# Performance work log

Measured on AMD Instinct MI355X. Metric: run time of the kernel, lower is better.

The kernel has to match this reference:

```python
import jax, jax.numpy as jnp
import numpy as np

LOG2PI = float(np.log(2.0 * np.pi))
CLIP_LO, CLIP_HI = 1e-6, 1.0 - 1e-6


def gaussian_log_prob(X, mu):
    # X: (s, d), mu: (K, d) -> (s, K); unit-variance diagonal Normal.
    d = X.shape[-1]
    sq = (
        (X * X).sum(-1, keepdims=True)
        - 2.0 * (X @ mu.T)
        + (mu * mu).sum(-1)[None, :]
    )
    return -0.5 * (sq + d * LOG2PI)


def setup_inputs() -> dict:
    key = jax.random.key(0)
    kz, ks, kd, km1, km2 = jax.random.split(key, 5)
    s, K, n, dz = 60000, 200, 6, 64
    Z = jax.random.normal(kz, (s, dz), dtype=jnp.float32)
    S = jax.random.normal(ks, (s, 3), dtype=jnp.float32)
    D = jax.random.randint(kd, (s, n), 0, s, dtype=jnp.int64)
    sel_mu = jax.random.normal(km1, (K, dz), dtype=jnp.float32)
    spa_mu = jax.random.normal(km2, (K, 3), dtype=jnp.float32)
    return {"Z": Z, "S": S, "D": D, "sel_mu": sel_mu, "spa_mu": spa_mu}


def reference(Z, S, D, sel_mu, spa_mu):
    # point energy U: (s, K)
    U = -(gaussian_log_prob(Z, sel_mu) + gaussian_log_prob(S, spa_mu))
    Q = jax.nn.softmax(-U, axis=-1)  # temperature = 1.0
    # expected point energy: (s,)
    point = (Q * U).sum(-1)
    # doublet energy: gather neighbor rows, coassignment, potential, mask
    Qc = jnp.clip(Q, CLIP_LO, CLIP_HI)
    co = jnp.einsum('snk,sk->sn', Qc[D], Qc)  # (s, n)
    doublet = jnp.where(D < 0, 0.0, -jnp.log(co)).sum(-1)  # (s,)
    return point + doublet
```

## Files before the change

kernel.cpp:

```cpp
#include <hip/hip_runtime.h>
#include <hip/hip_fp16.h>
#include <math.h>

#define KK 200
#define NT 13
#define NNB 6
#define Q8STRIDE 256

typedef __attribute__((ext_vector_type(8))) short short8;
typedef __attribute__((ext_vector_type(4))) float f32x4;
#define MFMA16 __builtin_amdgcn_mfma_f32_16x16x32_bf16

__device__ __forceinline__ unsigned short bfh(float f) {
    unsigned u = __float_as_uint(f);
    return (unsigned short)((u + 0x7fffu + ((u >> 16) & 1u)) >> 16);
}
__device__ __forceinline__ float bf2f(unsigned short h) {
    return __uint_as_float(((unsigned)h) << 16);
}
__device__ __forceinline__ short8 z8() {
    short8 v;
#pragma unroll
    for (int j = 0; j < 8; ++j) v[j] = 0;
    return v;
}
__device__ __forceinline__ void cv2(float f, short8& hi, short8& lo, int j) {
    unsigned short h = bfh(f);
    hi[j] = (short)h;
    lo[j] = (short)bfh(f - bf2f(h));
}
__device__ __forceinline__ unsigned f2e5(float f) {
    unsigned short hb = __half_as_ushort(__float2half(f));
    return (unsigned)((unsigned short)((hb + 0x7fu + ((hb >> 8) & 1u)) >> 8));
}
__device__ __forceinline__ void dec8(unsigned w, float* f) {
    f[0] = __half2float(__ushort_as_half((unsigned short)((w << 8) & 0xff00u)));
    f[1] = __half2float(__ushort_as_half((unsigned short)(w & 0xff00u)));
    f[2] = __half2float(__ushort_as_half((unsigned short)((w >> 8) & 0xff00u)));
    f[3] = __half2float(__ushort_as_half((unsigned short)((w >> 16) & 0xff00u)));
}

__global__ __launch_bounds__(512, 4) void
k_point(const float* __restrict__ Z, const float* __restrict__ S,
        const float* __restrict__ selmu, const float* __restrict__ spamu,
        unsigned char* __restrict__ Qc8, float* __restrict__ pointbuf,
        int sRows, int mTiles)
{
    __shared__ short8 ldsBh[26 * 64];
    __shared__ short8 ldsBl[26 * 64];
    __shared__ uint2  ldsB2h[NT * 16];
    __shared__ uint2  ldsB2l[NT * 16];

    const int tid = threadIdx.x;

    for (int slot = tid; slot < 26 * 64; slot += 512) {
        int L = slot & 63, ts = slot >> 6;
        int t = ts >> 1, sstep = ts & 1;
        int n = t * 16 + (L & 15);
        int kb = sstep * 32 + (L >> 4) * 8;
        short8 hi = z8(), lo = z8();
        if (n < KK) {
            const float* mp = selmu + (size_t)n * 64 + kb;
            float4 a = *(const float4*)mp;
            float4 b = *(const float4*)(mp + 4);
            cv2(a.x, hi, lo, 0); cv2(a.y, hi, lo, 1); cv2(a.z, hi, lo, 2); cv2(a.w, hi, lo, 3);
            cv2(b.x, hi, lo, 4); cv2(b.y, hi, lo, 5); cv2(b.z, hi, lo, 6); cv2(b.w, hi, lo, 7);
        }
        ldsBh[slot] = hi;
        ldsBl[slot] = lo;
    }
    if (tid < NT * 16) {
        int n = tid;
        uint2 vh = make_uint2(0, 0), vl = make_uint2(0, 0);
        if (n < KK) {
            float p0 = spamu[n * 3 + 0], p1 = spamu[n * 3 + 1], p2 = spamu[n * 3 + 2];
            float nrm = p0 * p0 + p1 * p1 + p2 * p2;
            const float* mp = selmu + (size_t)n * 64;
#pragma unroll 8
            for (int k = 0; k < 64; ++k) { float m = mp[k]; nrm = fmaf(m, m, nrm); }
            nrm *= -0.5f;
            unsigned short h0 = bfh(p0), h1 = bfh(p1), h2 = bfh(p2), h3 = bfh(nrm);
            unsigned short g0 = bfh(p0 - bf2f(h0)), g1 = bfh(p1 - bf2f(h1));
            unsigned short g2 = bfh(p2 - bf2f(h2)), g3 = bfh(nrm - bf2f(h3));
            vh = make_uint2((unsigned)h0 | ((unsigned)h1 << 16), (unsigned)h2 | ((unsigned)h3 << 16));
            vl = make_uint2((unsigned)g0 | ((unsigned)g1 << 16), (unsigned)g2 | ((unsigned)g3 << 16));
        }
        ldsB2h[tid] = vh;
        ldsB2l[tid] = vl;
    }
    __syncthreads();

    const int wave = tid >> 6;
    const int lane = tid & 63;
    const int q = lane >> 4;
    const int li = lane & 15;
    const float cLog = 0.5f * 67.0f * 1.8378770664093453f;

    const int tile = blockIdx.x * 8 + wave;
    if (tile >= mTiles) return;
    const int m0 = tile * 16;
    const int row = m0 + li;
    const int rowA = (row < sRows) ? row : (sRows - 1);

    const float* zr = Z + (size_t)rowA * 64 + q * 8;
    float4 z0 = *(const float4*)zr;
    float4 z1 = *(const float4*)(zr + 4);
    float4 z2 = *(const float4*)(zr + 32);
    float4 z3 = *(const float4*)(zr + 36);
    short8 ah0 = z8(), al0 = z8(), ah1 = z8(), al1 = z8();
    cv2(z0.x, ah0, al0, 0); cv2(z0.y, ah0, al0, 1); cv2(z0.z, ah0, al0, 2); cv2(z0.w, ah0, al0, 3);
    cv2(z1.x, ah0, al0, 4); cv2(z1.y, ah0, al0, 5); cv2(z1.z, ah0, al0, 6); cv2(z1.w, ah0, al0, 7);
    cv2(z2.x, ah1, al1, 0); cv2(z2.y, ah1, al1, 1); cv2(z2.z, ah1, al1, 2); cv2(z2.w, ah1, al1, 3);
    cv2(z3.x, ah1, al1, 4); cv2(z3.y, ah1, al1, 5); cv2(z3.z, ah1, al1, 6); cv2(z3.w, ah1, al1, 7);

    float zz = z0.x*z0.x + z0.y*z0.y + z0.z*z0.z + z0.w*z0.w
             + z1.x*z1.x + z1.y*z1.y + z1.z*z1.z + z1.w*z1.w
             + z2.x*z2.x + z2.y*z2.y + z2.z*z2.z + z2.w*z2.w
             + z3.x*z3.x + z3.y*z3.y + z3.z*z3.z + z3.w*z3.w;
    zz += __shfl_xor(zz, 16);
    zz += __shfl_xor(zz, 32);

    float s0v = S[(size_t)rowA * 3 + 0];
    float s1v = S[(size_t)rowA * 3 + 1];
    float s2v = S[(size_t)rowA * 3 + 2];
    float cz = 0.5f * (zz + s0v * s0v + s1v * s1v + s2v * s2v) + cLog;

    short8 rsh = z8(), rsl = z8();
    if (lane < 16) {
        cv2(s0v, rsh, rsl, 0);
        cv2(s1v, rsh, rsl, 1);
        cv2(s2v, rsh, rsl, 2);
        rsh[3] = (short)bfh(1.0f);
    }

    f32x4 acc[NT];
#pragma unroll
    for (int t = 0; t < NT; ++t) { f32x4 zv = {0.f, 0.f, 0.f, 0.f}; acc[t] = zv; }

#pragma unroll
    for (int t = 0; t < NT; ++t) {
        short8 b0 = ldsBh[(t * 2 + 0) * 64 + lane];
        short8 b1 = ldsBh[(t * 2 + 1) * 64 + lane];
        short8 c0 = ldsBl[(t * 2 + 0) * 64 + lane];
        short8 c1 = ldsBl[(t * 2 + 1) * 64 + lane];
        uint2 bh2 = make_uint2(0, 0), bl2 = make_uint2(0, 0);
        if (lane < 16) { bh2 = ldsB2h[t * 16 + lane]; bl2 = ldsB2l[t * 16 + lane]; }
        short8 cmh = z8(), cml = z8();
        cmh[0] = (short)(bh2.x & 0xffff); cmh[1] = (short)(bh2.x >> 16);
        cmh[2] = (short)(bh2.y & 0xffff); cmh[3] = (short)(bh2.y >> 16);
        cml[0] = (short)(bl2.x & 0xffff); cml[1] = (short)(bl2.x >> 16);
        cml[2] = (short)(bl2.y & 0xffff); cml[3] = (short)(bl2.y >> 16);

        acc[t] = MFMA16(b0, ah0, acc[t], 0, 0, 0);
        acc[t] = MFMA16(b1, ah1, acc[t], 0, 0, 0);
        acc[t] = MFMA16(b0, al0, acc[t], 0, 0, 0);
        acc[t] = MFMA16(b1, al1, acc[t], 0, 0, 0);
        acc[t] = MFMA16(c0, ah0, acc[t], 0, 0, 0);
        acc[t] = MFMA16(c1, ah1, acc[t], 0, 0, 0);
        acc[t] = MFMA16(cmh, rsh, acc[t], 0, 0, 0);
        acc[t] = MFMA16(cmh, rsl, acc[t], 0, 0, 0);
        acc[t] = MFMA16(cml, rsh, acc[t], 0, 0, 0);
    }

    const bool padQ = (q >= 2);
    float mx = -1e30f;
#pragma unroll
    for (int t = 0; t < NT; ++t) {
#pragma unroll
        for (int r = 0; r < 4; ++r) {
            float v = acc[t][r];
            if (t == 12 && padQ) v = -1e30f;
            acc[t][r] = v;
            mx = fmaxf(mx, v);
        }
    }
    mx = fmaxf(mx, __shfl_xor(mx, 16));
    mx = fmaxf(mx, __shfl_xor(mx, 32));
    float sl = 0.f, pl = 0.f;
#pragma unroll
    for (int t = 0; t < NT; ++t) {
#pragma unroll
        for (int r = 0; r < 4; ++r) {
            float v = acc[t][r];
            float ee = __expf(v - mx);
            sl += ee;
            pl = fmaf(ee, v, pl);
            acc[t][r] = ee;
        }
    }
    sl += __shfl_xor(sl, 16);
    sl += __shfl_xor(sl, 32);
    pl += __shfl_xor(pl, 16);
    pl += __shfl_xor(pl, 32);
    float inv = 1.0f / sl;

    if (row < sRows) {
        unsigned char* qp = Qc8 + (size_t)row * Q8STRIDE + q * 4;
#pragma unroll
        for (int t = 0; t < NT; ++t) {
            unsigned w = 0;
            if (t < 12 || !padQ) {
                float q0 = fminf(fmaxf(acc[t][0] * inv, 1e-6f), 1.0f - 1e-6f);
                float q1 = fminf(fmaxf(acc[t][1] * inv, 1e-6f), 1.0f - 1e-6f);
                float q2 = fminf(fmaxf(acc[t][2] * inv, 1e-6f), 1.0f - 1e-6f);
                float q3 = fminf(fmaxf(acc[t][3] * inv, 1e-6f), 1.0f - 1e-6f);
                w = f2e5(q0 * 1024.0f) | (f2e5(q1 * 1024.0f) << 8)
                  | (f2e5(q2 * 1024.0f) << 16) | (f2e5(q3 * 1024.0f) << 24);
            }
            *(unsigned*)(qp + t * 16) = w;
        }
        if (lane < 16) pointbuf[row] = cz - pl * inv;
    }
}

__global__ __launch_bounds__(512) void
k_doublet(const unsigned char* __restrict__ Qc8, const float* __restrict__ pointbuf,
          const int* __restrict__ D, float* __restrict__ out, int sRows, int mTiles)
{
    const int wave = threadIdx.x >> 6;
    const int lane = threadIdx.x & 63;
    const int half = lane >> 5;
    const int l = lane & 31;
    const int sub = blockIdx.x >> 9;
    const int b = blockIdx.x & 511;
    const int T = b * 8 + wave;
    if (T >= mTiles) return;
    const int rbase = T * 16 + sub * 8 + half;

    const bool act = (l < 25);
    const int lc = act ? l : 0;
    const float LN2_20 = 13.862943611198906f;

    int   dj0[NNB], dj1[NNB], dj2[NNB];
    uint2 nb0[NNB], nb1[NNB];
    uint2 ow0, ow1;
    {
        int rc0 = rbase,     c0 = (rc0 < sRows) ? rc0 : (sRows - 1);
        int rc1 = rbase + 2, c1 = (rc1 < sRows) ? rc1 : (sRows - 1);
#pragma unroll
        for (int j = 0; j < NNB; ++j) dj0[j] = D[(size_t)c0 * NNB + j];
#pragma unroll
        for (int j = 0; j < NNB; ++j) dj1[j] = D[(size_t)c1 * NNB + j];
        ow0 = *(const uint2*)(Qc8 + (size_t)c0 * Q8STRIDE + lc * 8);
        ow1 = *(const uint2*)(Qc8 + (size_t)c1 * Q8STRIDE + lc * 8);
#pragma unroll
        for (int j = 0; j < NNB; ++j) {
            int dd = (dj0[j] >= 0) ? dj0[j] : c0;
            nb0[j] = *(const uint2*)(Qc8 + (size_t)dd * Q8STRIDE + lc * 8);
        }
    }

    for (int it = 0; it < 4; ++it) {
        const int row = rbase + it * 2;
        if (it < 2) {
            int rc = rbase + (it + 2) * 2;
            int cc = (rc < sRows) ? rc : (sRows - 1);
#pragma unroll
            for (int j = 0; j < NNB; ++j) dj2[j] = D[(size_t)cc * NNB + j];
        }
        if (it < 3) {
            int rc = rbase + (it + 1) * 2;
            int cc = (rc < sRows) ? rc : (sRows - 1);
#pragma unroll
            for (int j = 0; j < NNB; ++j) {
                int dd = (dj1[j] >= 0) ? dj1[j] : cc;
                nb1[j] = *(const uint2*)(Qc8 + (size_t)dd * Q8STRIDE + lc * 8);
            }
        }

        float o[8];
        dec8(ow0.x, o);
        dec8(ow0.y, o + 4);
        float pj[NNB];
#pragma unroll
        for (int j = 0; j < NNB; ++j) {
            float bv[8];
            dec8(nb0[j].x, bv);
            dec8(nb0[j].y, bv + 4);
            float t = o[0] * bv[0];
            t = fmaf(o[1], bv[1], t); t = fmaf(o[2], bv[2], t); t = fmaf(o[3], bv[3], t);
            t = fmaf(o[4], bv[4], t); t = fmaf(o[5], bv[5], t); t = fmaf(o[6], bv[6], t);
            t = fmaf(o[7], bv[7], t);
            pj[j] = act ? t : 0.f;
        }
#pragma unroll
        for (int off = 1; off <= 16; off <<= 1) {
#pragma unroll
            for (int j = 0; j < NNB; ++j) pj[j] += __shfl_xor(pj[j], off);
        }
        float dbl = 0.f;
#pragma unroll
        for (int j = 0; j < NNB; ++j)
            if (dj0[j] >= 0) dbl += LN2_20 - __logf(pj[j]);

        if (l == 0 && row < sRows) out[row] = pointbuf[row] + dbl;

        ow0 = ow1;
        if (it < 2) {
            int rc = rbase + (it + 2) * 2;
            int cc = (rc < sRows) ? rc : (sRows - 1);
            ow1 = *(const uint2*)(Qc8 + (size_t)cc * Q8STRIDE + lc * 8);
        }
#pragma unroll
        for (int j = 0; j < NNB; ++j) { dj0[j] = dj1[j]; dj1[j] = dj2[j]; nb0[j] = nb1[j]; }
    }
}

extern "C" void kernel_launch(void* const* d_in, const int* in_sizes, int n_in,
                              void* d_out, int out_size, void* d_ws, size_t ws_size,
                              hipStream_t stream) {
    const float* Z     = (const float*)d_in[0];
    const float* S     = (const float*)d_in[1];
    const int*   D     = (const int*)d_in[2];
    const float* selmu = (const float*)d_in[3];
    const float* spamu = (const float*)d_in[4];
    float* out = (float*)d_out;
    const int s = out_size;

    unsigned char* Qc8 = (unsigned char*)d_ws;
    float* pointbuf = (float*)((char*)d_ws + (size_t)s * Q8STRIDE);

    const int mTiles = (s + 15) / 16;
    const int grid1 = (mTiles + 7) / 8;
    k_point<<<grid1, 512, 0, stream>>>(Z, S, selmu, spamu, Qc8, pointbuf, s, mTiles);

    k_doublet<<<1024, 512, 0, stream>>>(Qc8, pointbuf, D, out, s, mTiles);
}
```

Baseline: 108.0 us.

## Map one wave per row in doublet kernel, split neighbors across half-waves

Rewrites the doublet kernel so each wave handles a single row, with its two 32-lane halves each processing three of the six neighbors. The old persistent 1024-block grid, where each half-wave software-pipelined four rows, is replaced by a grid of one block per eight rows. The goal is more parallelism and more memory-level concurrency from many resident waves rather than manual prefetching, and it adds an occupancy hint to launch bounds. The cost is more blocks, a cross-half shuffle per row, and no explicit overlap of loads with compute.

```diff
diff --git a/kernel.cpp b/kernel.cpp
--- a/kernel.cpp
+++ b/kernel.cpp
@@ -213,97 +213,64 @@
     }
 }
 
-__global__ __launch_bounds__(512) void
+__global__ __launch_bounds__(512, 8) void
 k_doublet(const unsigned char* __restrict__ Qc8, const float* __restrict__ pointbuf,
-          const int* __restrict__ D, float* __restrict__ out, int sRows, int mTiles)
+          const int* __restrict__ D, float* __restrict__ out, int sRows)
 {
     const int wave = threadIdx.x >> 6;
     const int lane = threadIdx.x & 63;
     const int half = lane >> 5;
     const int l = lane & 31;
-    const int sub = blockIdx.x >> 9;
-    const int b = blockIdx.x & 511;
-    const int T = b * 8 + wave;
-    if (T >= mTiles) return;
-    const int rbase = T * 16 + sub * 8 + half;
+    const int row = blockIdx.x * 8 + wave;
+    if (row >= sRows) return;
 
     const bool act = (l < 25);
     const int lc = act ? l : 0;
     const float LN2_20 = 13.862943611198906f;
 
-    int   dj0[NNB], dj1[NNB], dj2[NNB];
-    uint2 nb0[NNB], nb1[NNB];
-    uint2 ow0, ow1;
-    {
-        int rc0 = rbase,     c0 = (rc0 < sRows) ? rc0 : (sRows - 1);
-        int rc1 = rbase + 2, c1 = (rc1 < sRows) ? rc1 : (sRows - 1);
-#pragma unroll
-        for (int j = 0; j < NNB; ++j) dj0[j] = D[(size_t)c0 * NNB + j];
-#pragma unroll
-        for (int j = 0; j < NNB; ++j) dj1[j] = D[(size_t)c1 * NNB + j];
-        ow0 = *(const uint2*)(Qc8 + (size_t)c0 * Q8STRIDE + lc * 8);
-        ow1 = *(const uint2*)(Qc8 + (size_t)c1 * Q8STRIDE + lc * 8);
-#pragma unroll
-        for (int j = 0; j < NNB; ++j) {
-            int dd = (dj0[j] >= 0) ? dj0[j] : c0;
-            nb0[j] = *(const uint2*)(Qc8 + (size_t)dd * Q8STRIDE + lc * 8);
-        }
-    }
-
-    for (int it = 0; it < 4; ++it) {
-        const int row = rbase + it * 2;
-        if (it < 2) {
-            int rc = rbase + (it + 2) * 2;
-            int cc = (rc < sRows) ? rc : (sRows - 1);
-#pragma unroll
-            for (int j = 0; j < NNB; ++j) dj2[j] = D[(size_t)cc * NNB + j];
-        }
-        if (it < 3) {
-            int rc = rbase + (it + 1) * 2;
-            int cc = (rc < sRows) ? rc : (sRows - 1);
-#pragma unroll
-            for (int j = 0; j < NNB; ++j) {
-                int dd = (dj1[j] >= 0) ? dj1[j] : cc;
-                nb1[j] = *(const uint2*)(Qc8 + (size_t)dd * Q8STRIDE + lc * 8);
-            }
-        }
-
-        float o[8];
-        dec8(ow0.x, o);
-        dec8(ow0.y, o + 4);
-        float pj[NNB];
-#pragma unroll
-        for (int j = 0; j < NNB; ++j) {
-            float bv[8];
-            dec8(nb0[j].x, bv);
-            dec8(nb0[j].y, bv + 4);
-            float t = o[0] * bv[0];
-            t = fmaf(o[1], bv[1], t); t = fmaf(o[2], bv[2], t); t = fmaf(o[3], bv[3], t);
-            t = fmaf(o[4], bv[4], t); t = fmaf(o[5], bv[5], t); t = fmaf(o[6], bv[6], t);
-            t = fmaf(o[7], bv[7], t);
-            pj[j] = act ? t : 0.f;
-        }
-#pragma unroll
-        for (int off = 1; off <= 16; off <<= 1) {
-#pragma unroll
-            for (int j = 0; j < NNB; ++j) pj[j] += __shfl_xor(pj[j], off);
-        }
-        float dbl = 0.f;
-#pragma unroll
-        for (int j = 0; j < NNB; ++j)
-            if (dj0[j] >= 0) dbl += LN2_20 - __logf(pj[j]);
-
-        if (l == 0 && row < sRows) out[row] = pointbuf[row] + dbl;
-
-        ow0 = ow1;
-        if (it < 2) {
-            int rc = rbase + (it + 2) * 2;
-            int cc = (rc < sRows) ? rc : (sRows - 1);
-            ow1 = *(const uint2*)(Qc8 + (size_t)cc * Q8STRIDE + lc * 8);
-        }
-#pragma unroll
-        for (int j = 0; j < NNB; ++j) { dj0[j] = dj1[j]; dj1[j] = dj2[j]; nb0[j] = nb1[j]; }
-    }
+    const int* dp = D + (size_t)row * NNB;
+    int da0 = dp[0], da1 = dp[1], da2 = dp[2], da3 = dp[3], da4 = dp[4], da5 = dp[5];
+    int dj[3];
+    dj[0] = half ? da1 : da0;
+    dj[1] = half ? da3 : da2;
+    dj[2] = half ? da5 : da4;
+
+    uint2 ow = *(const uint2*)(Qc8 + (size_t)row * Q8STRIDE + lc * 8);
+    uint2 nb[3];
+#pragma unroll
+    for (int i = 0; i < 3; ++i) {
+        int dd = (dj[i] >= 0) ? dj[i] : row;
+        nb[i] = *(const uint2*)(Qc8 + (size_t)dd * Q8STRIDE + lc * 8);
+    }
+
+    float o[8];
+    dec8(ow.x, o);
+    dec8(ow.y, o + 4);
+
+    float pj[3];
+#pragma unroll
+    for (int i = 0; i < 3; ++i) {
+        float bv[8];
+        dec8(nb[i].x, bv);
+        dec8(nb[i].y, bv + 4);
+        float t = o[0] * bv[0];
+        t = fmaf(o[1], bv[1], t); t = fmaf(o[2], bv[2], t); t = fmaf(o[3], bv[3], t);
+        t = fmaf(o[4], bv[4], t); t = fmaf(o[5], bv[5], t); t = fmaf(o[6], bv[6], t);
+        t = fmaf(o[7], bv[7], t);
+        pj[i] = act ? t : 0.f;
+    }
+#pragma unroll
+    for (int off = 1; off <= 16; off <<= 1) {
+#pragma unroll
+        for (int i = 0; i < 3; ++i) pj[i] += __shfl_xor(pj[i], off);
+    }
+    float dbl = 0.f;
+#pragma unroll
+    for (int i = 0; i < 3; ++i)
+        if (dj[i] >= 0) dbl += LN2_20 - __logf(pj[i]);
+    dbl += __shfl_xor(dbl, 32);
+
+    if (lane == 0) out[row] = pointbuf[row] + dbl;
 }
 
 extern "C" void kernel_launch(void* const* d_in, const int* in_sizes, int n_in,
@@ -324,5 +291,6 @@
     const int grid1 = (mTiles + 7) / 8;
     k_point<<<grid1, 512, 0, stream>>>(Z, S, selmu, spamu, Qc8, pointbuf, s, mTiles);
 
-    k_doublet<<<1024, 512, 0, stream>>>(Qc8, pointbuf, D, out, s, mTiles);
-}
+    const int grid2 = (s + 7) / 8;
+    k_doublet<<<grid2, 512, 0, stream>>>(Qc8, pointbuf, D, out, s);
+}
```

Result: no change. 107.5 us (-0.5%).
